# Kernel tuning notes

Measured on AMD Instinct MI355X. Metric: run time of the kernel, lower is better.

The kernel has to match this reference:

```python
import jax, jax.numpy as jnp
import numpy as np

B, N, C, L = 32, 1024, 1024, 16  # batch, pixels (HW), channels, visual tokens


def setup_inputs() -> dict:
    key = jax.random.key(0)
    ks = jax.random.split(key, 18)
    s = lambda fan_in: 1.0 / np.sqrt(fan_in)
    def lin(kw, kb, fin, fout):
        W = jax.random.uniform(kw, (fin, fout), jnp.float32, -s(fin), s(fin))
        b = jax.random.uniform(kb, (fout,), jnp.float32, -s(fin), s(fin))
        return W, b
    tok_W, tok_b = lin(ks[0], ks[1], C, L)          # tokenizer pointwise conv
    key_W, key_b = lin(ks[2], ks[3], C, C // 2)     # transformer key proj
    query_W, query_b = lin(ks[4], ks[5], C, C // 2) # transformer query proj
    f1_W, f1_b = lin(ks[6], ks[7], C, C)            # FFN 1
    f2_W, f2_b = lin(ks[8], ks[9], C, C)            # FFN 2
    q_W, q_b = lin(ks[10], ks[11], C, C)            # projector W_q
    k_W, k_b = lin(ks[12], ks[13], C, C)            # projector W_k
    feature_map = jax.random.normal(ks[14], (B, N, C), jnp.float32)
    T_in = jnp.zeros((B, L, C), jnp.float32)  # unused by FilterBasedTokenizer
    return dict(feature_map=feature_map, T_in=T_in,
                tok_W=tok_W, tok_b=tok_b, key_W=key_W, key_b=key_b,
                query_W=query_W, query_b=query_b, f1_W=f1_W, f1_b=f1_b,
                f2_W=f2_W, f2_b=f2_b, q_W=q_W, q_b=q_b, k_W=k_W, k_b=k_b)


def reference(feature_map, T_in, tok_W, tok_b, key_W, key_b, query_W, query_b,
              f1_W, f1_b, f2_W, f2_b, q_W, q_b, k_W, k_b):
    X = feature_map  # [B, N, C]
    # --- FilterBasedTokenizer: softmax over pixel dim, aggregate pixels -> tokens
    proj = X @ tok_W + tok_b                         # [B, N, L]
    attn = jax.nn.softmax(proj, axis=1)              # softmax over N (dim=1)
    T = jnp.einsum('bnl,bnc->blc', attn, X)          # [B, L, C]
    # --- Transformer block on visual tokens
    k = T @ key_W + key_b                            # [B, L, C/2]
    q = T @ query_W + query_b                        # [B, L, C/2]
    scores = jnp.einsum('bld,bmd->blm', k, q)        # [B, L, L]
    T_dash = T + jax.nn.softmax(scores, axis=2) @ T  # self-attn residual
    T_out = T_dash + (jax.nn.relu(T_dash @ f1_W + f1_b) @ f2_W + f2_b)
    # --- Projector: pixels attend to tokens
    sim = jnp.einsum('bnc,blc->bnl', X @ q_W + q_b, T_out @ k_W + k_b)  # [B, N, L]
    X_out = X + jax.nn.softmax(sim, axis=2) @ T_out  # [B, N, C]
    return (X_out, T_out)
```

## Files before the change

### kernel.cpp

```cpp
#include <hip/hip_runtime.h>
#include <hip/hip_bf16.h>
#include <stdint.h>

#define BB 32
#define NN 1024
#define CC 1024
#define LL 16

typedef __attribute__((ext_vector_type(4))) float f32x4;
typedef __attribute__((ext_vector_type(2))) float f32x2;
typedef __attribute__((ext_vector_type(8))) short short8;
typedef __attribute__((ext_vector_type(4))) unsigned short ushort4v;
typedef __attribute__((ext_vector_type(2))) unsigned short ushort2v;

__device__ __forceinline__ unsigned short f2bf(float f) {
  union { float f; unsigned u; } v; v.f = f;
  unsigned r = v.u + 0x7FFF + ((v.u >> 16) & 1);
  return (unsigned short)(r >> 16);
}
__device__ __forceinline__ float bf2f(unsigned short h) {
  union { unsigned u; float f; } v; v.u = ((unsigned)h) << 16; return v.f;
}
__device__ __forceinline__ short8 cvt8(f32x4 a, f32x4 b) {
  short8 r;
  r[0] = (short)f2bf(a[0]); r[1] = (short)f2bf(a[1]);
  r[2] = (short)f2bf(a[2]); r[3] = (short)f2bf(a[3]);
  r[4] = (short)f2bf(b[0]); r[5] = (short)f2bf(b[1]);
  r[6] = (short)f2bf(b[2]); r[7] = (short)f2bf(b[3]);
  return r;
}

__global__ __launch_bounds__(256) void tokprep(
    const float* __restrict__ tokW, const float* __restrict__ keyb,
    const float* __restrict__ queryb,
    unsigned short* __restrict__ tokWT, float* __restrict__ biaskq)
{
  int gid = blockIdx.x * 256 + threadIdx.x;
  if (gid < 16384) {
    int l = gid >> 10, c = gid & 1023;
    tokWT[gid] = f2bf(tokW[c * 16 + l]);
  } else if (gid < 17408) {
    int i = gid - 16384;
    biaskq[i] = (i < 512) ? keyb[i] : queryb[i - 512];
  }
}

__global__ __launch_bounds__(512) void tok_fused(
    const float* __restrict__ X, const unsigned short* __restrict__ tokWT,
    const float* __restrict__ tokB, unsigned short* __restrict__ Tp,
    float* __restrict__ Mloc, float* __restrict__ Sloc,
    const float* __restrict__ keyW, const float* __restrict__ queryW,
    const float* __restrict__ f1W, const float* __restrict__ f2W,
    const float* __restrict__ kW, const float* __restrict__ qW,
    unsigned short* __restrict__ WkqT, unsigned short* __restrict__ f1WT,
    unsigned short* __restrict__ f2WT, unsigned short* __restrict__ kWT,
    unsigned short* __restrict__ qWbf)
{
  __shared__ float E[64][16];
  __shared__ __align__(16) f32x4 accbuf[4][64];
  __shared__ float redm[4][16], reds[4][16];
  int tid = threadIdx.x;
  if (blockIdx.x >= 16) {
    int prep_id = (blockIdx.x - 16) * 32 + blockIdx.y;
    int tx = tid & 31, ty = tid >> 5;
    __shared__ float tile[32][33];
    for (int i = 0; i < 32; ++i) {
      int t = prep_id * 32 + i;
      int z = t >> 10, idx = t & 1023;
      int j0 = (idx & 31) * 32, k0 = (idx >> 5) * 32;
      if (z == 4) {
#pragma unroll
        for (int q = 0; q < 2; ++q) {
          int row = k0 + ty + 16 * q, col = j0 + tx;
          qWbf[row * 1024 + col] = f2bf(qW[row * 1024 + col]);
        }
      } else {
        const float* src = (z == 1) ? f1W : (z == 2) ? f2W : kW;
#pragma unroll
        for (int q = 0; q < 2; ++q) {
          int k = k0 + ty + 16 * q, j = j0 + tx;
          float v;
          if (z == 0) v = (j < 512) ? keyW[k * 512 + j] : queryW[k * 512 + (j - 512)];
          else        v = src[k * 1024 + j];
          tile[ty + 16 * q][tx] = v;
        }
        __syncthreads();
        unsigned short* dst = (z == 0) ? WkqT : (z == 1) ? f1WT : (z == 2) ? f2WT : kWT;
#pragma unroll
        for (int q = 0; q < 2; ++q) {
          int j = j0 + ty + 16 * q;
          dst[j * 1024 + k0 + tx] = f2bf(tile[tx][ty + 16 * q]);
        }
        __syncthreads();
      }
    }
    return;
  }
  int wid = tid >> 6, lane = tid & 63;
  int lr = lane & 15, hi = lane >> 4;
  int rowgrp = wid & 3, khalf = wid >> 2;
  int b = blockIdx.y, ch = blockIdx.x;
  int pix0 = b * 1024 + ch * 64;
  const float* Ar = X + (size_t)(pix0 + rowgrp * 16 + lr) * 1024 + khalf * 512 + hi * 8;
  const unsigned short* Br = tokWT + lr * 1024 + khalf * 512 + hi * 8;
  f32x4 acc = (f32x4)0.f;
#pragma unroll 8
  for (int k0 = 0; k0 < 512; k0 += 32) {
    f32x4 x0 = *(const f32x4*)(Ar + k0);
    f32x4 x1 = *(const f32x4*)(Ar + k0 + 4);
    short8 bfrag = *(const short8*)(Br + k0);
    acc = __builtin_amdgcn_mfma_f32_16x16x32_bf16(cvt8(x0, x1), bfrag, acc, 0, 0, 0);
  }
  if (khalf == 1) accbuf[rowgrp][lane] = acc;
  __syncthreads();
  float tb = tokB[lr];
  float sv[4];
  if (khalf == 0) {
    f32x4 other = accbuf[rowgrp][lane];
#pragma unroll
    for (int rr = 0; rr < 4; ++rr) sv[rr] = acc[rr] + other[rr] + tb;
    float pm = fmaxf(fmaxf(sv[0], sv[1]), fmaxf(sv[2], sv[3]));
    pm = fmaxf(pm, __shfl_xor(pm, 16));
    pm = fmaxf(pm, __shfl_xor(pm, 32));
    if (hi == 0) redm[rowgrp][lr] = pm;
  }
  __syncthreads();
  if (khalf == 0) {
    float m = fmaxf(fmaxf(redm[0][lr], redm[1][lr]), fmaxf(redm[2][lr], redm[3][lr]));
    float ev[4]; float ps = 0.f;
#pragma unroll
    for (int i = 0; i < 4; ++i) { ev[i] = __expf(sv[i] - m); ps += ev[i]; }
    ps += __shfl_xor(ps, 16); ps += __shfl_xor(ps, 32);
    if (hi == 0) reds[rowgrp][lr] = ps;
#pragma unroll
    for (int rr = 0; rr < 4; ++rr)
      E[rowgrp * 16 + hi * 4 + rr][lr] = ev[rr];
    if (wid == 0 && hi == 0) {
    }
  }
  __syncthreads();
  if (tid < 16) {
    float m2 = fmaxf(fmaxf(redm[0][tid], redm[1][tid]), fmaxf(redm[2][tid], redm[3][tid]));
    float sl = reds[0][tid] + reds[1][tid] + reds[2][tid] + reds[3][tid];
    Mloc[(b * 16 + ch) * 16 + tid] = m2;
    Sloc[(b * 16 + ch) * 16 + tid] = sl;
  }
  f32x2 a16[16];
#pragma unroll
  for (int l = 0; l < 16; ++l) a16[l] = (f32x2)0.f;
  const float* xp = X + (size_t)pix0 * 1024 + tid * 2;
  for (int n0 = 0; n0 < 64; n0 += 8) {
    f32x2 xv[8];
#pragma unroll
    for (int i = 0; i < 8; ++i) xv[i] = *(const f32x2*)(xp + (size_t)(n0 + i) * 1024);
#pragma unroll
    for (int i = 0; i < 8; ++i) {
      const f32x4* ar = (const f32x4*)&E[n0 + i][0];
      f32x4 a0 = ar[0], a1 = ar[1], a2 = ar[2], a3 = ar[3];
      f32x2 x0 = xv[i];
      a16[0]  += a0[0]*x0; a16[1]  += a0[1]*x0; a16[2]  += a0[2]*x0; a16[3]  += a0[3]*x0;
      a16[4]  += a1[0]*x0; a16[5]  += a1[1]*x0; a16[6]  += a1[2]*x0; a16[7]  += a1[3]*x0;
      a16[8]  += a2[0]*x0; a16[9]  += a2[1]*x0; a16[10] += a2[2]*x0; a16[11] += a2[3]*x0;
      a16[12] += a3[0]*x0; a16[13] += a3[1]*x0; a16[14] += a3[2]*x0; a16[15] += a3[3]*x0;
    }
  }
  unsigned short* op = Tp + ((size_t)(b * 16 + ch) * 16) * 1024 + tid * 2;
#pragma unroll
  for (int l = 0; l < 16; ++l) {
    f32x2 s = a16[l];
    ushort2v h; h[0] = f2bf(s[0]); h[1] = f2bf(s[1]);
    *(ushort2v*)(op + (size_t)l * 1024) = h;
  }
}

__global__ __launch_bounds__(256) void tmerge(
    const unsigned short* __restrict__ Tp, const float* __restrict__ Mloc,
    const float* __restrict__ Sloc, float* __restrict__ T,
    unsigned short* __restrict__ Tbf)
{
  int tid = threadIdx.x;
  int g = blockIdx.x * 2 + (tid >> 7);
  int b = g >> 4, l = g & 15;
  int j = tid & 127;
  float M = -1e30f;
#pragma unroll
  for (int ch = 0; ch < 16; ++ch) M = fmaxf(M, Mloc[(b * 16 + ch) * 16 + l]);
  float w[16]; float denom = 0.f;
#pragma unroll
  for (int ch = 0; ch < 16; ++ch) {
    w[ch] = __expf(Mloc[(b * 16 + ch) * 16 + l] - M);
    denom += w[ch] * Sloc[(b * 16 + ch) * 16 + l];
  }
  float inv = 1.f / denom;
  float o[8];
#pragma unroll
  for (int t = 0; t < 8; ++t) o[t] = 0.f;
#pragma unroll
  for (int ch = 0; ch < 16; ++ch) {
    const unsigned short* p = Tp + ((size_t)((b * 16 + ch) * 16 + l)) * 1024 + j * 8;
    short8 v = *(const short8*)p;
    float wc = w[ch];
#pragma unroll
    for (int t = 0; t < 8; ++t) o[t] += wc * bf2f((unsigned short)v[t]);
  }
  f32x4 o0, o1; short8 hb;
#pragma unroll
  for (int t = 0; t < 4; ++t) {
    float x0 = o[t] * inv, x1 = o[4 + t] * inv;
    o0[t] = x0; o1[t] = x1;
    hb[t] = (short)f2bf(x0); hb[4 + t] = (short)f2bf(x1);
  }
  *(f32x4*)(T + (size_t)g * 1024 + j * 8) = o0;
  *(f32x4*)(T + (size_t)g * 1024 + j * 8 + 4) = o1;
  *(short8*)(Tbf + (size_t)g * 1024 + j * 8) = hb;
}

template<int RELU, int HAS_BIAS, int HAS_RES, int STORE_F32, int STORE_BF16>
__global__ __launch_bounds__(256) void gemm32x64(
    const unsigned short* __restrict__ A, const unsigned short* __restrict__ Bm,
    const float* __restrict__ bias, const float* __restrict__ res,
    float* __restrict__ outF, unsigned short* __restrict__ outB)
{
  const int K = 1024;
  __shared__ __align__(16) char sh[12288];
  char* Asp = sh;
  char* Bsp = sh + 4096;
  int tid = threadIdx.x, wid = tid >> 6, lane = tid & 63;
  int lr = lane & 15, hi = lane >> 4;
  int m0 = blockIdx.x * 32, n0 = blockIdx.y * 64;
  int arow = tid >> 3, acol = (tid & 7) * 8;
  int brow = tid >> 2, bcol = (tid & 3) * 16;
  const unsigned short* Ap = A + (size_t)(m0 + arow) * K + acol;
  const unsigned short* Bp = Bm + (size_t)(n0 + brow) * K + bcol;
  int aw  = arow * 128 + (((acol * 2) ^ ((arow & 7) << 4)));
  int bw0 = brow * 128 + (((bcol * 2) ^ ((brow & 7) << 4)));
  int bw1 = brow * 128 + ((((bcol * 2) + 16) ^ ((brow & 7) << 4)));
  short8 aR[4]; short8 bR[4][2];
#pragma unroll
  for (int p = 0; p < 4; ++p) {
    aR[p]    = *(const short8*)(Ap + p * 64);
    bR[p][0] = *(const short8*)(Bp + p * 64);
    bR[p][1] = *(const short8*)(Bp + p * 64 + 8);
  }
  f32x4 acc[2];
  acc[0] = (f32x4)0.f; acc[1] = (f32x4)0.f;
  int wm = (wid >> 1) * 16, wn = (wid & 1) * 32;
  int arb = (wm + lr) * 128, arx = ((wm + lr) & 7) << 4;
  for (int s = 0; s < 16; ++s) {
    __syncthreads();
    *(short8*)(Asp + aw)  = aR[s & 3];
    *(short8*)(Bsp + bw0) = bR[s & 3][0];
    *(short8*)(Bsp + bw1) = bR[s & 3][1];
    __syncthreads();
    if (s + 4 < 16) {
      int k0 = (s + 4) * 64;
      aR[s & 3]    = *(const short8*)(Ap + k0);
      bR[s & 3][0] = *(const short8*)(Bp + k0);
      bR[s & 3][1] = *(const short8*)(Bp + k0 + 8);
    }
#pragma unroll
    for (int kk = 0; kk < 2; ++kk) {
      short8 af = *(const short8*)(Asp + arb + (((kk * 64 + hi * 16) ^ arx)));
#pragma unroll
      for (int sn = 0; sn < 2; ++sn) {
        int br = wn + sn * 16 + lr;
        short8 bf = *(const short8*)(Bsp + br * 128 + (((kk * 64 + hi * 16) ^ ((br & 7) << 4))));
        acc[sn] = __builtin_amdgcn_mfma_f32_16x16x32_bf16(af, bf, acc[sn], 0, 0, 0);
      }
    }
  }
  int row0 = m0 + wm + hi * 4;
#pragma unroll
  for (int sn = 0; sn < 2; ++sn) {
    int col = n0 + wn + sn * 16 + lr;
    float bv_ = HAS_BIAS ? bias[col] : 0.f;
#pragma unroll
    for (int rr = 0; rr < 4; ++rr) {
      float x = acc[sn][rr] + bv_;
      if (RELU) x = fmaxf(x, 0.f);
      size_t idx = (size_t)(row0 + rr) * 1024 + col;
      if (HAS_RES) x += res[idx];
      if (STORE_F32) outF[idx] = x;
      if (STORE_BF16) outB[idx] = f2bf(x);
    }
  }
}

__global__ __launch_bounds__(256) void scores_tdash(
    const float* __restrict__ kq, const float* __restrict__ T,
    float* __restrict__ Tdash, unsigned short* __restrict__ Tdbf)
{
  int cs = blockIdx.x, b = blockIdx.y;
  int c0 = cs * 128;
  __shared__ float Ts[16][128];
  int tid = threadIdx.x, lane = tid & 63;
#pragma unroll
  for (int i = 0; i < 2; ++i) {
    int fi = tid + 256 * i;
    int rrow = fi >> 5, c4 = (fi & 31) * 4;
    *(f32x4*)&Ts[rrow][c4] = *(const f32x4*)&T[((size_t)b * 16 + rrow) * 1024 + c0 + c4];
  }
  __syncthreads();
  int l = tid >> 4, m = tid & 15;
  const float* krow = kq + ((size_t)b * 16 + l) * 1024;
  const float* qrow = kq + ((size_t)b * 16 + m) * 1024 + 512;
  float s = 0.f;
#pragma unroll 8
  for (int d = 0; d < 512; d += 4) {
    f32x4 kv = *(const f32x4*)(krow + d);
    f32x4 qv = *(const f32x4*)(qrow + d);
    s += kv[0]*qv[0] + kv[1]*qv[1] + kv[2]*qv[2] + kv[3]*qv[3];
  }
  float mx = s;
  mx = fmaxf(mx, __shfl_xor(mx, 1)); mx = fmaxf(mx, __shfl_xor(mx, 2));
  mx = fmaxf(mx, __shfl_xor(mx, 4)); mx = fmaxf(mx, __shfl_xor(mx, 8));
  float e = __expf(s - mx);
  float sum = e;
  sum += __shfl_xor(sum, 1); sum += __shfl_xor(sum, 2);
  sum += __shfl_xor(sum, 4); sum += __shfl_xor(sum, 8);
  float pv = e / sum;
  float pl[16];
#pragma unroll
  for (int i = 0; i < 16; ++i) pl[i] = __shfl(pv, (lane & 48) + i);
  float* od = Tdash + ((size_t)b * 16 + l) * 1024 + c0;
  unsigned short* ob = Tdbf + ((size_t)b * 16 + l) * 1024 + c0;
#pragma unroll
  for (int h = 0; h < 2; ++h) {
    int c = m * 8 + h * 4;
    f32x4 o = *(const f32x4*)&Ts[l][c];
#pragma unroll
    for (int mm = 0; mm < 16; ++mm) {
      f32x4 tv = *(const f32x4*)&Ts[mm][c];
      o += pl[mm] * tv;
    }
    *(f32x4*)(od + c) = o;
    ushort4v hh; hh[0]=f2bf(o[0]); hh[1]=f2bf(o[1]); hh[2]=f2bf(o[2]); hh[3]=f2bf(o[3]);
    *(ushort4v*)(ob + c) = hh;
  }
}

__global__ __launch_bounds__(256) void r_kernel(
    const unsigned short* __restrict__ Tkbf, const float* __restrict__ qb,
    float* __restrict__ r)
{
  int row = blockIdx.x * 4 + (threadIdx.x >> 6);
  int lane = threadIdx.x & 63;
  const unsigned short* p = Tkbf + (size_t)row * CC;
  float s = 0.f;
#pragma unroll
  for (int h = 0; h < 2; ++h) {
    int d0 = lane * 8 + h * 512;
    short8 v = *(const short8*)&p[d0];
#pragma unroll
    for (int jj = 0; jj < 8; ++jj)
      s += bf2f((unsigned short)v[jj]) * qb[d0 + jj];
  }
#pragma unroll
  for (int msk = 32; msk >= 1; msk >>= 1) s += __shfl_xor(s, msk);
  if (lane == 0) r[row] = s;
}

__global__ __launch_bounds__(512) void sim_out_kernel(
    const float* __restrict__ X, const unsigned short* __restrict__ Gt,
    const float* __restrict__ rbias, const float* __restrict__ Tout,
    float* __restrict__ Xout)
{
  __shared__ float Ps[64][16];
  __shared__ __align__(16) f32x4 accbuf[4][64];
  int tid = threadIdx.x, wid = tid >> 6, lane = tid & 63;
  int lr = lane & 15, hi = lane >> 4;
  int rowgrp = wid & 3, khalf = wid >> 2;
  int b = blockIdx.y;
  int pix0 = b * 1024 + blockIdx.x * 64;
  const float* Ar = X + (size_t)(pix0 + rowgrp * 16 + lr) * 1024 + khalf * 512 + hi * 8;
  const unsigned short* Br = Gt + (size_t)b * 16384 + lr * 1024 + khalf * 512 + hi * 8;
  f32x4 acc = (f32x4)0.f;
#pragma unroll 8
  for (int k0 = 0; k0 < 512; k0 += 32) {
    f32x4 x0 = *(const f32x4*)(Ar + k0);
    f32x4 x1 = *(const f32x4*)(Ar + k0 + 4);
    short8 bfrag = *(const short8*)(Br + k0);
    acc = __builtin_amdgcn_mfma_f32_16x16x32_bf16(cvt8(x0, x1), bfrag, acc, 0, 0, 0);
  }
  if (khalf == 1) accbuf[rowgrp][lane] = acc;
  __syncthreads();
  if (khalf == 0) {
    f32x4 other = accbuf[rowgrp][lane];
    float bv = rbias[b * 16 + lr];
    int prow = rowgrp * 16 + hi * 4;
#pragma unroll
    for (int rr = 0; rr < 4; ++rr) {
      float vv = acc[rr] + other[rr] + bv;
      float mx = vv;
      mx = fmaxf(mx, __shfl_xor(mx, 1)); mx = fmaxf(mx, __shfl_xor(mx, 2));
      mx = fmaxf(mx, __shfl_xor(mx, 4)); mx = fmaxf(mx, __shfl_xor(mx, 8));
      float e = __expf(vv - mx);
      float ss = e;
      ss += __shfl_xor(ss, 1); ss += __shfl_xor(ss, 2);
      ss += __shfl_xor(ss, 4); ss += __shfl_xor(ss, 8);
      Ps[prow + rr][lr] = e / ss;
    }
  }
  __syncthreads();
  int half = tid >> 8, tn = tid & 255;
  int c4 = tn * 4;
  f32x4 tsr[16];
#pragma unroll
  for (int l = 0; l < 16; ++l)
    tsr[l] = *(const f32x4*)&Tout[((size_t)b * 16 + l) * 1024 + c4];
  const float* xp = X + (size_t)(pix0 + half * 32) * 1024 + c4;
  float* op = Xout + (size_t)(pix0 + half * 32) * 1024 + c4;
#pragma unroll 2
  for (int n = 0; n < 32; ++n) {
    f32x4 xv = *(const f32x4*)(xp + (size_t)n * 1024);
    const f32x4* pr = (const f32x4*)&Ps[half * 32 + n][0];
    f32x4 p0 = pr[0], p1 = pr[1], p2 = pr[2], p3 = pr[3];
    f32x4 o = xv;
    o += p0[0]*tsr[0];  o += p0[1]*tsr[1];  o += p0[2]*tsr[2];  o += p0[3]*tsr[3];
    o += p1[0]*tsr[4];  o += p1[1]*tsr[5];  o += p1[2]*tsr[6];  o += p1[3]*tsr[7];
    o += p2[0]*tsr[8];  o += p2[1]*tsr[9];  o += p2[2]*tsr[10]; o += p2[3]*tsr[11];
    o += p3[0]*tsr[12]; o += p3[1]*tsr[13]; o += p3[2]*tsr[14]; o += p3[3]*tsr[15];
    __builtin_nontemporal_store(o, (f32x4*)(op + (size_t)n * 1024));
  }
}

extern "C" void kernel_launch(void* const* d_in, const int* in_sizes, int n_in,
                              void* d_out, int out_size, void* d_ws, size_t ws_size,
                              hipStream_t stream)
{
  const float* X      = (const float*)d_in[0];
  const float* tokW   = (const float*)d_in[2];
  const float* tokB   = (const float*)d_in[3];
  const float* keyW   = (const float*)d_in[4];
  const float* keyB   = (const float*)d_in[5];
  const float* queryW = (const float*)d_in[6];
  const float* queryB = (const float*)d_in[7];
  const float* f1W    = (const float*)d_in[8];
  const float* f1B    = (const float*)d_in[9];
  const float* f2W    = (const float*)d_in[10];
  const float* f2B    = (const float*)d_in[11];
  const float* qW     = (const float*)d_in[12];
  const float* qB     = (const float*)d_in[13];
  const float* kW     = (const float*)d_in[14];
  const float* kB     = (const float*)d_in[15];

  float* Xout = (float*)d_out;
  float* Tout = (float*)d_out + (size_t)BB * NN * CC;

  char* ws = (char*)d_ws;
  size_t off = 0;
  auto alloc_f = [&](size_t n) { float* pp = (float*)(ws + off); off += n * 4; return pp; };
  float* Tbuf   = alloc_f(524288);
  float* kqbuf  = alloc_f(524288);
  float* Tdash  = alloc_f(524288);
  float* rbuf   = alloc_f(1024);
  float* biaskq = alloc_f(1024);
  float* Mloc   = alloc_f(8192);
  float* Sloc   = alloc_f(8192);
  auto alloc_h = [&](size_t n) { unsigned short* pp = (unsigned short*)(ws + off); off += n * 2; return pp; };
  unsigned short* Tp     = alloc_h(8388608);
  unsigned short* Tbf    = alloc_h(524288);
  unsigned short* Tdbf   = alloc_h(524288);
  unsigned short* Hbf    = alloc_h(524288);
  unsigned short* Toutbf = alloc_h(524288);
  unsigned short* Tkbf   = alloc_h(524288);
  unsigned short* Gtbf   = alloc_h(524288);
  unsigned short* WkqT   = alloc_h(1048576);
  unsigned short* f1WT   = alloc_h(1048576);
  unsigned short* f2WT   = alloc_h(1048576);
  unsigned short* kWT    = alloc_h(1048576);
  unsigned short* qWbf   = alloc_h(1048576);
  unsigned short* tokWT  = alloc_h(16384);
  (void)ws_size; (void)in_sizes; (void)n_in; (void)out_size;

  tokprep<<<68, 256, 0, stream>>>(tokW, keyB, queryB, tokWT, biaskq);
  tok_fused<<<dim3(21, 32), 512, 0, stream>>>(X, tokWT, tokB, Tp, Mloc, Sloc,
                                              keyW, queryW, f1W, f2W, kW, qW,
                                              WkqT, f1WT, f2WT, kWT, qWbf);
  tmerge<<<256, 256, 0, stream>>>(Tp, Mloc, Sloc, Tbuf, Tbf);
  gemm32x64<0,1,0,1,0><<<dim3(16, 16), 256, 0, stream>>>(Tbf, WkqT, biaskq, nullptr, kqbuf, nullptr);
  scores_tdash<<<dim3(8, 32), 256, 0, stream>>>(kqbuf, Tbuf, Tdash, Tdbf);
  gemm32x64<1,1,0,0,1><<<dim3(16, 16), 256, 0, stream>>>(Tdbf, f1WT, f1B, nullptr, nullptr, Hbf);
  gemm32x64<0,1,1,1,1><<<dim3(16, 16), 256, 0, stream>>>(Hbf, f2WT, f2B, Tdash, Tout, Toutbf);
  gemm32x64<0,1,0,0,1><<<dim3(16, 16), 256, 0, stream>>>(Toutbf, kWT, kB, nullptr, nullptr, Tkbf);
  r_kernel<<<128, 256, 0, stream>>>(Tkbf, qB, rbuf);
  gemm32x64<0,0,0,0,1><<<dim3(16, 16), 256, 0, stream>>>(Tkbf, qWbf, nullptr, nullptr, nullptr, Gtbf);
  sim_out_kernel<<<dim3(16, 32), 512, 0, stream>>>(X, Gtbf, rbuf, Tout, Xout);
}
```

Measured before the change: 185.7 us.

## Split weight prep into dedicated kernel and widen tokenizer aggregation per thread

Weight transposition and bf16 conversion move out of the tokenizer kernel into a separate wide-grid prep kernel, which also absorbs the old tokprep launch. Previously 160 blocks each looped serially over 32 tiles alongside the tokenizer. The tokenizer's pixel-aggregation phase now has each thread handle 4 channels over half the pixels. The two halves are combined through shared memory, which adds an extra bf16 rounding of the partial sum. Occupancy hints are added via launch_bounds on the tokenizer and output kernels, at some risk of register pressure from the larger accumulator array.

```diff
diff --git a/kernel.cpp b/kernel.cpp
--- a/kernel.cpp
+++ b/kernel.cpp
@@ -8,10 +8,8 @@
 #define LL 16
 
 typedef __attribute__((ext_vector_type(4))) float f32x4;
-typedef __attribute__((ext_vector_type(2))) float f32x2;
 typedef __attribute__((ext_vector_type(8))) short short8;
 typedef __attribute__((ext_vector_type(4))) unsigned short ushort4v;
-typedef __attribute__((ext_vector_type(2))) unsigned short ushort2v;
 
 __device__ __forceinline__ unsigned short f2bf(float f) {
   union { float f; unsigned u; } v; v.f = f;
@@ -30,72 +28,70 @@
   return r;
 }
 
-__global__ __launch_bounds__(256) void tokprep(
-    const float* __restrict__ tokW, const float* __restrict__ keyb,
-    const float* __restrict__ queryb,
-    unsigned short* __restrict__ tokWT, float* __restrict__ biaskq)
-{
-  int gid = blockIdx.x * 256 + threadIdx.x;
-  if (gid < 16384) {
-    int l = gid >> 10, c = gid & 1023;
-    tokWT[gid] = f2bf(tokW[c * 16 + l]);
-  } else if (gid < 17408) {
-    int i = gid - 16384;
-    biaskq[i] = (i < 512) ? keyb[i] : queryb[i - 512];
-  }
-}
-
-__global__ __launch_bounds__(512) void tok_fused(
-    const float* __restrict__ X, const unsigned short* __restrict__ tokWT,
-    const float* __restrict__ tokB, unsigned short* __restrict__ Tp,
-    float* __restrict__ Mloc, float* __restrict__ Sloc,
+__global__ __launch_bounds__(256) void wprep(
     const float* __restrict__ keyW, const float* __restrict__ queryW,
     const float* __restrict__ f1W, const float* __restrict__ f2W,
     const float* __restrict__ kW, const float* __restrict__ qW,
+    const float* __restrict__ tokW, const float* __restrict__ keyb,
+    const float* __restrict__ queryb,
     unsigned short* __restrict__ WkqT, unsigned short* __restrict__ f1WT,
     unsigned short* __restrict__ f2WT, unsigned short* __restrict__ kWT,
-    unsigned short* __restrict__ qWbf)
+    unsigned short* __restrict__ qWbf, unsigned short* __restrict__ tokWT,
+    float* __restrict__ biaskq)
+{
+  int z = blockIdx.z;
+  int tx = threadIdx.x, ty = threadIdx.y;
+  if (z == 5) {
+    int gid = (blockIdx.y * 32 + blockIdx.x) * 256 + ty * 32 + tx;
+    if (gid < 16384) {
+      int l = gid >> 10, c = gid & 1023;
+      tokWT[gid] = f2bf(tokW[c * 16 + l]);
+    } else if (gid < 17408) {
+      int i = gid - 16384;
+      biaskq[i] = (i < 512) ? keyb[i] : queryb[i - 512];
+    }
+    return;
+  }
+  if (z == 4) {
+#pragma unroll
+    for (int i = 0; i < 4; ++i) {
+      int row = blockIdx.y * 32 + ty + 8 * i;
+      int col = blockIdx.x * 32 + tx;
+      qWbf[row * 1024 + col] = f2bf(qW[row * 1024 + col]);
+    }
+    return;
+  }
+  __shared__ float tile[32][33];
+  int j0 = blockIdx.x * 32, k0 = blockIdx.y * 32;
+  const float* src = (z == 1) ? f1W : (z == 2) ? f2W : kW;
+#pragma unroll
+  for (int i = 0; i < 4; ++i) {
+    int k = k0 + ty + 8 * i;
+    int j = j0 + tx;
+    float v;
+    if (z == 0) v = (j < 512) ? keyW[k * 512 + j] : queryW[k * 512 + (j - 512)];
+    else        v = src[k * 1024 + j];
+    tile[ty + 8 * i][tx] = v;
+  }
+  __syncthreads();
+  unsigned short* dst = (z == 0) ? WkqT : (z == 1) ? f1WT : (z == 2) ? f2WT : kWT;
+#pragma unroll
+  for (int i = 0; i < 4; ++i) {
+    int j = j0 + ty + 8 * i;
+    dst[j * 1024 + k0 + tx] = f2bf(tile[tx][ty + 8 * i]);
+  }
+}
+
+__global__ __launch_bounds__(512, 4) void tok_fused(
+    const float* __restrict__ X, const unsigned short* __restrict__ tokWT,
+    const float* __restrict__ tokB, unsigned short* __restrict__ Tp,
+    float* __restrict__ Mloc, float* __restrict__ Sloc)
 {
   __shared__ float E[64][16];
   __shared__ __align__(16) f32x4 accbuf[4][64];
   __shared__ float redm[4][16], reds[4][16];
+  __shared__ __align__(16) ushort4v hbuf[256][16];
   int tid = threadIdx.x;
-  if (blockIdx.x >= 16) {
-    int prep_id = (blockIdx.x - 16) * 32 + blockIdx.y;
-    int tx = tid & 31, ty = tid >> 5;
-    __shared__ float tile[32][33];
-    for (int i = 0; i < 32; ++i) {
-      int t = prep_id * 32 + i;
-      int z = t >> 10, idx = t & 1023;
-      int j0 = (idx & 31) * 32, k0 = (idx >> 5) * 32;
-      if (z == 4) {
-#pragma unroll
-        for (int q = 0; q < 2; ++q) {
-          int row = k0 + ty + 16 * q, col = j0 + tx;
-          qWbf[row * 1024 + col] = f2bf(qW[row * 1024 + col]);
-        }
-      } else {
-        const float* src = (z == 1) ? f1W : (z == 2) ? f2W : kW;
-#pragma unroll
-        for (int q = 0; q < 2; ++q) {
-          int k = k0 + ty + 16 * q, j = j0 + tx;
-          float v;
-          if (z == 0) v = (j < 512) ? keyW[k * 512 + j] : queryW[k * 512 + (j - 512)];
-          else        v = src[k * 1024 + j];
-          tile[ty + 16 * q][tx] = v;
-        }
-        __syncthreads();
-        unsigned short* dst = (z == 0) ? WkqT : (z == 1) ? f1WT : (z == 2) ? f2WT : kWT;
-#pragma unroll
-        for (int q = 0; q < 2; ++q) {
-          int j = j0 + ty + 16 * q;
-          dst[j * 1024 + k0 + tx] = f2bf(tile[tx][ty + 16 * q]);
-        }
-        __syncthreads();
-      }
-    }
-    return;
-  }
   int wid = tid >> 6, lane = tid & 63;
   int lr = lane & 15, hi = lane >> 4;
   int rowgrp = wid & 3, khalf = wid >> 2;
@@ -135,8 +131,6 @@
 #pragma unroll
     for (int rr = 0; rr < 4; ++rr)
       E[rowgrp * 16 + hi * 4 + rr][lr] = ev[rr];
-    if (wid == 0 && hi == 0) {
-    }
   }
   __syncthreads();
   if (tid < 16) {
@@ -145,31 +139,47 @@
     Mloc[(b * 16 + ch) * 16 + tid] = m2;
     Sloc[(b * 16 + ch) * 16 + tid] = sl;
   }
-  f32x2 a16[16];
-#pragma unroll
-  for (int l = 0; l < 16; ++l) a16[l] = (f32x2)0.f;
-  const float* xp = X + (size_t)pix0 * 1024 + tid * 2;
-  for (int n0 = 0; n0 < 64; n0 += 8) {
-    f32x2 xv[8];
-#pragma unroll
-    for (int i = 0; i < 8; ++i) xv[i] = *(const f32x2*)(xp + (size_t)(n0 + i) * 1024);
+  int half = tid >> 8, tn = tid & 255;
+  int c4 = tn * 4;
+  f32x4 a16[16];
+#pragma unroll
+  for (int l = 0; l < 16; ++l) a16[l] = (f32x4)0.f;
+  const float* xp = X + (size_t)(pix0 + half * 32) * 1024 + c4;
+  for (int n0 = 0; n0 < 32; n0 += 8) {
+    f32x4 xv[8];
+#pragma unroll
+    for (int i = 0; i < 8; ++i) xv[i] = *(const f32x4*)(xp + (size_t)(n0 + i) * 1024);
 #pragma unroll
     for (int i = 0; i < 8; ++i) {
-      const f32x4* ar = (const f32x4*)&E[n0 + i][0];
+      const f32x4* ar = (const f32x4*)&E[half * 32 + n0 + i][0];
       f32x4 a0 = ar[0], a1 = ar[1], a2 = ar[2], a3 = ar[3];
-      f32x2 x0 = xv[i];
+      f32x4 x0 = xv[i];
       a16[0]  += a0[0]*x0; a16[1]  += a0[1]*x0; a16[2]  += a0[2]*x0; a16[3]  += a0[3]*x0;
       a16[4]  += a1[0]*x0; a16[5]  += a1[1]*x0; a16[6]  += a1[2]*x0; a16[7]  += a1[3]*x0;
       a16[8]  += a2[0]*x0; a16[9]  += a2[1]*x0; a16[10] += a2[2]*x0; a16[11] += a2[3]*x0;
       a16[12] += a3[0]*x0; a16[13] += a3[1]*x0; a16[14] += a3[2]*x0; a16[15] += a3[3]*x0;
     }
   }
-  unsigned short* op = Tp + ((size_t)(b * 16 + ch) * 16) * 1024 + tid * 2;
-#pragma unroll
-  for (int l = 0; l < 16; ++l) {
-    f32x2 s = a16[l];
-    ushort2v h; h[0] = f2bf(s[0]); h[1] = f2bf(s[1]);
-    *(ushort2v*)(op + (size_t)l * 1024) = h;
+  if (half == 1) {
+#pragma unroll
+    for (int l = 0; l < 16; ++l) {
+      f32x4 s = a16[l];
+      ushort4v h; h[0]=f2bf(s[0]); h[1]=f2bf(s[1]); h[2]=f2bf(s[2]); h[3]=f2bf(s[3]);
+      hbuf[tn][l] = h;
+    }
+  }
+  __syncthreads();
+  if (half == 0) {
+    unsigned short* op = Tp + ((size_t)(b * 16 + ch) * 16) * 1024 + c4;
+#pragma unroll
+    for (int l = 0; l < 16; ++l) {
+      ushort4v hv = hbuf[tn][l];
+      f32x4 s = a16[l];
+      s[0] += bf2f(hv[0]); s[1] += bf2f(hv[1]);
+      s[2] += bf2f(hv[2]); s[3] += bf2f(hv[3]);
+      ushort4v h; h[0]=f2bf(s[0]); h[1]=f2bf(s[1]); h[2]=f2bf(s[2]); h[3]=f2bf(s[3]);
+      *(ushort4v*)(op + (size_t)l * 1024) = h;
+    }
   }
 }
 
@@ -360,7 +370,7 @@
   if (lane == 0) r[row] = s;
 }
 
-__global__ __launch_bounds__(512) void sim_out_kernel(
+__global__ __launch_bounds__(512, 4) void sim_out_kernel(
     const float* __restrict__ X, const unsigned short* __restrict__ Gt,
     const float* __restrict__ rbias, const float* __restrict__ Tout,
     float* __restrict__ Xout)
@@ -473,10 +483,10 @@
   unsigned short* tokWT  = alloc_h(16384);
   (void)ws_size; (void)in_sizes; (void)n_in; (void)out_size;
 
-  tokprep<<<68, 256, 0, stream>>>(tokW, keyB, queryB, tokWT, biaskq);
-  tok_fused<<<dim3(21, 32), 512, 0, stream>>>(X, tokWT, tokB, Tp, Mloc, Sloc,
-                                              keyW, queryW, f1W, f2W, kW, qW,
-                                              WkqT, f1WT, f2WT, kWT, qWbf);
+  wprep<<<dim3(32, 32, 6), dim3(32, 8), 0, stream>>>(keyW, queryW, f1W, f2W, kW, qW,
+                                                     tokW, keyB, queryB,
+                                                     WkqT, f1WT, f2WT, kWT, qWbf, tokWT, biaskq);
+  tok_fused<<<dim3(16, 32), 512, 0, stream>>>(X, tokWT, tokB, Tp, Mloc, Sloc);
   tmerge<<<256, 256, 0, stream>>>(Tp, Mloc, Sloc, Tbuf, Tbf);
   gemm32x64<0,1,0,1,0><<<dim3(16, 16), 256, 0, stream>>>(Tbf, WkqT, biaskq, nullptr, kqbuf, nullptr);
   scores_tdash<<<dim3(8, 32), 256, 0, stream>>>(kqbuf, Tbuf, Tdash, Tdbf);
```

Result: slower. 206.4 us (+11.1%).
